# Kernel tuning notes

Hardware: AMD Instinct MI355X
Metric: run time of the kernel (lower is better)

Reference implementation:

```python
import jax, jax.numpy as jnp
import numpy as np

DIM = 1024
N_HEADS = 16
WINDOW = 256
B, N = 16, 4096
ACC = 512
EPS = 1e-5


def setup_inputs() -> dict:
    key = jax.random.key(0)
    ks = jax.random.split(key, 16)
    D = DIM
    sc = 1.0 / np.sqrt(D)
    inp = {
        "x": jax.random.normal(ks[0], (B, N, D), dtype=jnp.float32),
        "state": jax.random.normal(ks[1], (B, D), dtype=jnp.float32),
        "acc_ctx": jax.random.normal(ks[2], (B, ACC, D), dtype=jnp.float32),
        "fix_pt": jax.random.randint(ks[3], (B,), 0, N, dtype=jnp.int32),
        # MultiheadAttention params (torch layout: in_proj_weight [3D, D])
        "in_proj_w": jax.random.normal(ks[4], (3 * D, D), dtype=jnp.float32) * sc,
        "in_proj_b": jnp.zeros((3 * D,), dtype=jnp.float32),
        "out_w": jax.random.normal(ks[5], (D, D), dtype=jnp.float32) * sc,
        "out_b": jnp.zeros((D,), dtype=jnp.float32),
        # LayerNorms
        "ln1_g": jnp.ones((D,), dtype=jnp.float32),
        "ln1_b": jnp.zeros((D,), dtype=jnp.float32),
        "ln2_g": jnp.ones((D,), dtype=jnp.float32),
        "ln2_b": jnp.zeros((D,), dtype=jnp.float32),
        # FFN: dim -> 4*dim -> dim (stored so that y = x @ w + b)
        "w1": jax.random.normal(ks[6], (D, 4 * D), dtype=jnp.float32) * sc,
        "b1": jnp.zeros((4 * D,), dtype=jnp.float32),
        "w2": jax.random.normal(ks[7], (4 * D, D), dtype=jnp.float32) * (1.0 / np.sqrt(4 * D)),
        "b2": jnp.zeros((D,), dtype=jnp.float32),
    }
    return inp


def _layer_norm(x, g, b):
    m = jnp.mean(x, axis=-1, keepdims=True)
    v = jnp.mean(jnp.square(x - m), axis=-1, keepdims=True)
    return (x - m) * jax.lax.rsqrt(v + EPS) * g + b


def _extract_windows(x, fix_pt):
    # Vectorized equivalent of the per-sample python loop. For even window_size
    # and N >= window_size the original logic reduces to a clamped start index.
    half = WINDOW // 2
    n = x.shape[1]
    start = jnp.clip(fix_pt - half, 0, n - WINDOW)  # [B]
    idx = start[:, None] + jnp.arange(WINDOW)       # [B, W]
    return jnp.take_along_axis(x, idx[:, :, None], axis=1)  # [B, W, D]


def _mha(xq, in_proj_w, in_proj_b, out_w, out_b):
    # torch nn.MultiheadAttention self-attention, batch_first
    Bq, L, D = xq.shape
    hd = D // N_HEADS
    qkv = xq @ in_proj_w.T + in_proj_b                     # [B, L, 3D]
    q, k, v = jnp.split(qkv, 3, axis=-1)
    def heads(t):
        return t.reshape(Bq, L, N_HEADS, hd).transpose(0, 2, 1, 3)  # [B,H,L,hd]
    q, k, v = heads(q), heads(k), heads(v)
    scores = jnp.einsum('bhqd,bhkd->bhqk', q, k) / np.sqrt(hd)
    attn = jax.nn.softmax(scores, axis=-1)
    o = jnp.einsum('bhqk,bhkd->bhqd', attn, v)             # [B,H,L,hd]
    o = o.transpose(0, 2, 1, 3).reshape(Bq, L, D)
    return o @ out_w.T + out_b


def reference(x, state, acc_ctx, in_proj_w, in_proj_b, out_w, out_b,
              ln1_g, ln1_b, ln2_g, ln2_b, w1, b1, w2, b2, fix_pt):
    window = _extract_windows(x, fix_pt)                   # [B, W, D]
    cls = state[:, None, :]                                # [B, 1, D]
    ctx = jnp.concatenate([cls, acc_ctx, window], axis=1)  # [B, 1+A+W, D]
    normed = _layer_norm(ctx, ln1_g, ln1_b)
    out = _mha(normed, in_proj_w, in_proj_b, out_w, out_b)
    ctx = ctx + out
    cls_out = ctx[:, 0]
    h = jax.nn.gelu(_layer_norm(cls_out, ln2_g, ln2_b) @ w1 + b1, approximate=False)
    cls_out = cls_out + h @ w2 + b2
    new_acc = jnp.concatenate([acc_ctx, window], axis=1)
    return cls_out, new_acc
```

## Files before the change

kernel.cpp:

```cpp
#include <hip/hip_runtime.h>
#include <hip/hip_bf16.h>
#include <math.h>

#define DIM 1024
#define NHEADS 16
#define HD 64
#define WIN 256
#define NB 16
#define NSEQ 4096
#define NACC 512
#define LCTX 769
#define MROWS 12304
#define MPAD2 12544

typedef short bf16x8 __attribute__((ext_vector_type(8)));
typedef float f32x4 __attribute__((ext_vector_type(4)));

__device__ inline unsigned short f2b(float f) {
    union { float f; unsigned int u; } c; c.f = f;
    unsigned int u = c.u;
    u += 0x7FFFu + ((u >> 16) & 1u);
    return (unsigned short)(u >> 16);
}
__device__ inline float b2f(unsigned short h) {
    union { unsigned int u; float f; } c; c.u = ((unsigned int)h) << 16;
    return c.f;
}

__global__ __launch_bounds__(256) void build_ln_kernel(
    const float* __restrict__ x, const float* __restrict__ state,
    const float* __restrict__ acc_ctx, const int* __restrict__ fix_pt,
    const float* __restrict__ ln1_g, const float* __restrict__ ln1_b,
    const float* __restrict__ in_proj_w, unsigned short* __restrict__ Wb,
    unsigned short* __restrict__ normed, float* __restrict__ ctx0,
    float* __restrict__ newacc)
{
    int bid = blockIdx.x;
    int t = threadIdx.x;
    if (bid >= MPAD2) {
        int idx = (bid - MPAD2) * 256 + t;
        float4 v = ((const float4*)in_proj_w)[idx];
        ushort4 o;
        o.x = f2b(v.x); o.y = f2b(v.y); o.z = f2b(v.z); o.w = f2b(v.w);
        ((ushort4*)Wb)[idx] = o;
        return;
    }
    if (bid >= MROWS) {
        ushort4 z = make_ushort4(0, 0, 0, 0);
        ((ushort4*)(normed + (size_t)bid * DIM))[t] = z;
        return;
    }
    int b = bid / LCTX;
    int r = bid - b * LCTX;
    const float* src;
    if (r == 0) {
        src = state + (size_t)b * DIM;
    } else if (r <= NACC) {
        src = acc_ctx + ((size_t)b * NACC + (r - 1)) * DIM;
    } else {
        int fp = fix_pt[b];
        int start = fp - WIN / 2;
        if (start < 0) start = 0;
        if (start > NSEQ - WIN) start = NSEQ - WIN;
        src = x + ((size_t)b * NSEQ + start + (r - 1 - NACC)) * DIM;
    }
    float4 v = ((const float4*)src)[t];
    float s = v.x + v.y + v.z + v.w;
    float ss = v.x * v.x + v.y * v.y + v.z * v.z + v.w * v.w;
#pragma unroll
    for (int o = 32; o > 0; o >>= 1) { s += __shfl_down(s, o); ss += __shfl_down(ss, o); }
    __shared__ float rs[4], rss[4];
    int wid = t >> 6, lane = t & 63;
    if (lane == 0) { rs[wid] = s; rss[wid] = ss; }
    __syncthreads();
    float sum = rs[0] + rs[1] + rs[2] + rs[3];
    float sq  = rss[0] + rss[1] + rss[2] + rss[3];
    float mean = sum * (1.0f / DIM);
    float var = sq * (1.0f / DIM) - mean * mean;
    float rstd = rsqrtf(var + 1e-5f);
    float4 g  = ((const float4*)ln1_g)[t];
    float4 be = ((const float4*)ln1_b)[t];
    ushort4 nb;
    nb.x = f2b((v.x - mean) * rstd * g.x + be.x);
    nb.y = f2b((v.y - mean) * rstd * g.y + be.y);
    nb.z = f2b((v.z - mean) * rstd * g.z + be.z);
    nb.w = f2b((v.w - mean) * rstd * g.w + be.w);
    ((ushort4*)(normed + (size_t)bid * DIM))[t] = nb;
    if (r == 0) {
        ((float4*)(ctx0 + (size_t)b * DIM))[t] = v;
    } else {
        ((float4*)(newacc + ((size_t)b * (LCTX - 1) + (r - 1)) * DIM))[t] = v;
    }
}

__device__ inline void stage_half(const unsigned short* __restrict__ g,
                                  unsigned short* l, int t)
{
    {
        int r = t >> 3, c8 = (t & 7) ^ (r & 7);
        __builtin_amdgcn_global_load_lds(
            (const __attribute__((address_space(1))) void*)(g + (size_t)r * 1024 + c8 * 8),
            (__attribute__((address_space(3))) void*)(l + (size_t)t * 8), 16, 0, 0);
    }
    {
        int t2 = t + 512;
        int r = t2 >> 3, c8 = (t2 & 7) ^ (r & 7);
        __builtin_amdgcn_global_load_lds(
            (const __attribute__((address_space(1))) void*)(g + (size_t)r * 1024 + c8 * 8),
            (__attribute__((address_space(3))) void*)(l + (size_t)t2 * 8), 16, 0, 0);
    }
}

__device__ inline bf16x8 ldsw(const unsigned short* h, int r, int c8)
{
    int slot = r * 8 + (c8 ^ (r & 7));
    return *(const bf16x8*)(h + slot * 8);
}

__global__ __launch_bounds__(512, 2) void k_gemm8_kernel(
    const unsigned short* __restrict__ A,
    const unsigned short* __restrict__ Bw,
    const float* __restrict__ bias,
    unsigned short* __restrict__ C)
{
    __shared__ unsigned short sh[2][2][2][128 * 64];
    const int mt = blockIdx.x, nt = blockIdx.y;
    const int t = threadIdx.x;
    const int wid = t >> 6, lane = t & 63;
    const int wm = wid >> 2, wn = wid & 3;
    const int l15 = lane & 15, l16 = lane >> 4;
    const int rB = (wn & 1) * 64;
    const unsigned short* Abase = A + (size_t)mt * 256 * 1024;
    const unsigned short* Bbase = Bw + (size_t)nt * 256 * 1024;

    f32x4 acc[8][4] = {};
    bf16x8 a[4][2], b[4][2];

    stage_half(Abase,                   &sh[0][0][0][0], t);
    stage_half(Abase + 128 * 1024,      &sh[0][0][1][0], t);
    stage_half(Bbase,                   &sh[0][1][0][0], t);
    stage_half(Bbase + 128 * 1024,      &sh[0][1][1][0], t);
    stage_half(Bbase + 64,              &sh[1][1][0][0], t);
    stage_half(Bbase + 128 * 1024 + 64, &sh[1][1][1][0], t);
    asm volatile("s_waitcnt vmcnt(4)" ::: "memory");
    __builtin_amdgcn_s_barrier();

    auto ktile = [&](int T, bool stA, bool stB, bool steady) {
        const int d = T & 1;
        const unsigned short* AH = &sh[d][0][wm][0];
        const unsigned short* BH = &sh[d][1][wn >> 1][0];
        const int kA = (T + 1) * 64;
        const int kB = (T + 2) * 64;

#pragma unroll
        for (int i = 0; i < 4; ++i) {
            a[i][0] = ldsw(AH, i * 16 + l15, l16);
            a[i][1] = ldsw(AH, i * 16 + l15, 4 + l16);
        }
#pragma unroll
        for (int j = 0; j < 2; ++j) {
            b[j][0] = ldsw(BH, rB + j * 16 + l15, l16);
            b[j][1] = ldsw(BH, rB + j * 16 + l15, 4 + l16);
        }
        if (stA) stage_half(Abase + kA, &sh[d ^ 1][0][0][0], t);
        __builtin_amdgcn_sched_barrier(0);
        __builtin_amdgcn_s_barrier();
        asm volatile("s_waitcnt lgkmcnt(0)" ::: "memory");
        __builtin_amdgcn_sched_barrier(0);
        __builtin_amdgcn_s_setprio(1);
#pragma unroll
        for (int i = 0; i < 4; ++i)
#pragma unroll
            for (int j = 0; j < 2; ++j) {
                acc[i][j] = __builtin_amdgcn_mfma_f32_16x16x32_bf16(a[i][0], b[j][0], acc[i][j], 0, 0, 0);
                acc[i][j] = __builtin_amdgcn_mfma_f32_16x16x32_bf16(a[i][1], b[j][1], acc[i][j], 0, 0, 0);
            }
        __builtin_amdgcn_s_setprio(0);
        __builtin_amdgcn_sched_barrier(0);
        __builtin_amdgcn_s_barrier();

#pragma unroll
        for (int j = 2; j < 4; ++j) {
            b[j][0] = ldsw(BH, rB + j * 16 + l15, l16);
            b[j][1] = ldsw(BH, rB + j * 16 + l15, 4 + l16);
        }
        if (stA) stage_half(Abase + 128 * 1024 + kA, &sh[d ^ 1][0][1][0], t);
        __builtin_amdgcn_sched_barrier(0);
        __builtin_amdgcn_s_barrier();
        asm volatile("s_waitcnt lgkmcnt(0)" ::: "memory");
        __builtin_amdgcn_sched_barrier(0);
        __builtin_amdgcn_s_setprio(1);
#pragma unroll
        for (int i = 0; i < 4; ++i)
#pragma unroll
            for (int j = 2; j < 4; ++j) {
                acc[i][j] = __builtin_amdgcn_mfma_f32_16x16x32_bf16(a[i][0], b[j][0], acc[i][j], 0, 0, 0);
                acc[i][j] = __builtin_amdgcn_mfma_f32_16x16x32_bf16(a[i][1], b[j][1], acc[i][j], 0, 0, 0);
            }
        __builtin_amdgcn_s_setprio(0);
        __builtin_amdgcn_sched_barrier(0);
        __builtin_amdgcn_s_barrier();

#pragma unroll
        for (int i = 0; i < 4; ++i) {
            a[i][0] = ldsw(AH, 64 + i * 16 + l15, l16);
            a[i][1] = ldsw(AH, 64 + i * 16 + l15, 4 + l16);
        }
        if (stB) stage_half(Bbase + kB, &sh[d][1][0][0], t);
        __builtin_amdgcn_sched_barrier(0);
        __builtin_amdgcn_s_barrier();
        asm volatile("s_waitcnt lgkmcnt(0)" ::: "memory");
        __builtin_amdgcn_sched_barrier(0);
        __builtin_amdgcn_s_setprio(1);
#pragma unroll
        for (int i = 0; i < 4; ++i)
#pragma unroll
            for (int j = 0; j < 2; ++j) {
                acc[4 + i][j] = __builtin_amdgcn_mfma_f32_16x16x32_bf16(a[i][0], b[j][0], acc[4 + i][j], 0, 0, 0);
                acc[4 + i][j] = __builtin_amdgcn_mfma_f32_16x16x32_bf16(a[i][1], b[j][1], acc[4 + i][j], 0, 0, 0);
            }
        __builtin_amdgcn_s_setprio(0);
        __builtin_amdgcn_sched_barrier(0);
        __builtin_amdgcn_s_barrier();

        if (stB) stage_half(Bbase + 128 * 1024 + kB, &sh[d][1][1][0], t);
        __builtin_amdgcn_sched_barrier(0);
        __builtin_amdgcn_s_barrier();
        asm volatile("s_waitcnt lgkmcnt(0)" ::: "memory");
        __builtin_amdgcn_sched_barrier(0);
        __builtin_amdgcn_s_setprio(1);
#pragma unroll
        for (int i = 0; i < 4; ++i)
#pragma unroll
            for (int j = 2; j < 4; ++j) {
                acc[4 + i][j] = __builtin_amdgcn_mfma_f32_16x16x32_bf16(a[i][0], b[j][0], acc[4 + i][j], 0, 0, 0);
                acc[4 + i][j] = __builtin_amdgcn_mfma_f32_16x16x32_bf16(a[i][1], b[j][1], acc[4 + i][j], 0, 0, 0);
            }
        __builtin_amdgcn_s_setprio(0);
        if (steady) {
            asm volatile("s_waitcnt vmcnt(4)" ::: "memory");
        } else {
            asm volatile("s_waitcnt vmcnt(0)" ::: "memory");
        }
        __builtin_amdgcn_sched_barrier(0);
        __builtin_amdgcn_s_barrier();
    };

    for (int T = 0; T < 14; ++T) ktile(T, true, true, true);
    ktile(14, true, false, false);
    ktile(15, false, false, false);

#pragma unroll
    for (int i = 0; i < 8; ++i) {
        int gmb = mt * 256 + wm * 128 + i * 16 + l16 * 4;
#pragma unroll
        for (int j = 0; j < 4; ++j) {
            int gn = nt * 256 + wn * 64 + j * 16 + l15;
            float bs = bias[gn];
#pragma unroll
            for (int r = 0; r < 4; ++r) {
                int gm = gmb + r;
                if (gm < MROWS) C[(size_t)gm * 1024 + gn] = f2b(acc[i][j][r] + bs);
            }
        }
    }
}

__global__ __launch_bounds__(512) void attn3_kernel(
    const unsigned short* __restrict__ normed,
    const unsigned short* __restrict__ Wqb, const float* __restrict__ in_proj_w,
    const float* __restrict__ in_proj_b,
    const unsigned short* __restrict__ kb, float* __restrict__ o_all)
{
    int b = blockIdx.x & 15, h = blockIdx.x >> 4;
    int t = threadIdx.x;
    int wave = t >> 6, lane = t & 63;
    __shared__ float qs[64];
    __shared__ float sc[LCTX];
    __shared__ float red1[8], red2[8];
    __shared__ float c4[4][1024];
    __shared__ float cfin[1024];

    {
        const unsigned short* nr = normed + (size_t)(b * LCTX) * DIM;
        bf16x8 n0 = *(const bf16x8*)(nr + lane * 16);
        bf16x8 n1 = *(const bf16x8*)(nr + lane * 16 + 8);
#pragma unroll
        for (int jj = 0; jj < 8; ++jj) {
            int d = wave * 8 + jj;
            const unsigned short* wr = Wqb + (size_t)(h * 64 + d) * DIM;
            bf16x8 w0 = *(const bf16x8*)(wr + lane * 16);
            bf16x8 w1 = *(const bf16x8*)(wr + lane * 16 + 8);
            float s = 0.f;
#pragma unroll
            for (int u = 0; u < 8; ++u)
                s += b2f((unsigned short)n0[u]) * b2f((unsigned short)w0[u]);
#pragma unroll
            for (int u = 0; u < 8; ++u)
                s += b2f((unsigned short)n1[u]) * b2f((unsigned short)w1[u]);
#pragma unroll
            for (int o = 32; o > 0; o >>= 1) s += __shfl_down(s, o);
            if (lane == 0) qs[d] = s + in_proj_b[h * 64 + d];
        }
    }
    __syncthreads();

    float lmax = -1e30f;
    for (int l = t; l < LCTX; l += 512) {
        const unsigned short* kr = kb + ((size_t)(b * LCTX + l)) * 1024 + h * 64;
        const uint4* k4 = (const uint4*)kr;
        float s = 0.f;
#pragma unroll
        for (int c = 0; c < 8; ++c) {
            uint4 u = k4[c];
            s += qs[c * 8 + 0] * b2f((unsigned short)(u.x & 0xffffu));
            s += qs[c * 8 + 1] * b2f((unsigned short)(u.x >> 16));
            s += qs[c * 8 + 2] * b2f((unsigned short)(u.y & 0xffffu));
            s += qs[c * 8 + 3] * b2f((unsigned short)(u.y >> 16));
            s += qs[c * 8 + 4] * b2f((unsigned short)(u.z & 0xffffu));
            s += qs[c * 8 + 5] * b2f((unsigned short)(u.z >> 16));
            s += qs[c * 8 + 6] * b2f((unsigned short)(u.w & 0xffffu));
            s += qs[c * 8 + 7] * b2f((unsigned short)(u.w >> 16));
        }
        s *= 0.125f;
        sc[l] = s;
        lmax = fmaxf(lmax, s);
    }
#pragma unroll
    for (int o = 32; o > 0; o >>= 1) lmax = fmaxf(lmax, __shfl_down(lmax, o));
    if (lane == 0) red1[wave] = lmax;
    __syncthreads();
    float m = red1[0];
#pragma unroll
    for (int w8 = 1; w8 < 8; ++w8) m = fmaxf(m, red1[w8]);

    float lsum = 0.f;
    for (int l = t; l < LCTX; l += 512) {
        float p = __expf(sc[l] - m);
        sc[l] = p;
        lsum += p;
    }
#pragma unroll
    for (int o = 32; o > 0; o >>= 1) lsum += __shfl_down(lsum, o);
    if (lane == 0) red2[wave] = lsum;
    __syncthreads();
    float S = 0.f;
#pragma unroll
    for (int w8 = 0; w8 < 8; ++w8) S += red2[w8];

    const unsigned short* nb_ = normed + (size_t)(b * LCTX) * DIM;
    int oc = t & 127;
    int rg = t >> 7;
    float ca[8] = {};
    for (int l = rg; l < LCTX; l += 4) {
        bf16x8 v = *(const bf16x8*)(nb_ + (size_t)l * DIM + oc * 8);
        float p = sc[l];
#pragma unroll
        for (int u = 0; u < 8; ++u) ca[u] += p * b2f((unsigned short)v[u]);
    }
#pragma unroll
    for (int u = 0; u < 8; ++u) c4[rg][oc * 8 + u] = ca[u];
    __syncthreads();
    for (int k = t; k < 1024; k += 512)
        cfin[k] = c4[0][k] + c4[1][k] + c4[2][k] + c4[3][k];
    __syncthreads();

    float rS = 1.0f / S;
#pragma unroll
    for (int dd = 0; dd < 8; ++dd) {
        int d = wave * 8 + dd;
        const float* wr = in_proj_w + (size_t)(2048 + h * 64 + d) * DIM;
        float s = 0.f;
#pragma unroll
        for (int kk = 0; kk < 16; ++kk) {
            int k = kk * 64 + lane;
            s += wr[k] * cfin[k];
        }
#pragma unroll
        for (int o = 32; o > 0; o >>= 1) s += __shfl_down(s, o);
        if (lane == 0)
            o_all[b * 1024 + h * 64 + d] = s * rS + in_proj_b[2048 + h * 64 + d];
    }
}

__global__ __launch_bounds__(256) void out_proj_kernel(
    const float* __restrict__ o_all, const float* __restrict__ out_w,
    const float* __restrict__ out_b, const float* __restrict__ ctx0,
    float* __restrict__ cls_pre)
{
    int gw = blockIdx.x * 4 + (threadIdx.x >> 6);
    int lane = threadIdx.x & 63;
    int b = gw >> 10, i = gw & 1023;
    const float* orow = o_all + (size_t)b * 1024;
    const float* wrow = out_w + (size_t)i * 1024;
    float s = 0.f;
#pragma unroll
    for (int kk = 0; kk < 16; ++kk) {
        int k = kk * 64 + lane;
        s += orow[k] * wrow[k];
    }
#pragma unroll
    for (int o = 32; o > 0; o >>= 1) s += __shfl_down(s, o);
    if (lane == 0) cls_pre[gw] = ctx0[gw] + s + out_b[i];
}

__global__ __launch_bounds__(256) void ln2_kernel(
    const float* __restrict__ cls_pre, const float* __restrict__ g,
    const float* __restrict__ be, const float* __restrict__ b2,
    float* __restrict__ ln2o, float* __restrict__ outp)
{
    int b = blockIdx.x, t = threadIdx.x;
    float4 v = ((const float4*)(cls_pre + (size_t)b * DIM))[t];
    float s = v.x + v.y + v.z + v.w;
    float ss = v.x * v.x + v.y * v.y + v.z * v.z + v.w * v.w;
#pragma unroll
    for (int o = 32; o > 0; o >>= 1) { s += __shfl_down(s, o); ss += __shfl_down(ss, o); }
    __shared__ float rs[4], rss[4];
    int wid = t >> 6, lane = t & 63;
    if (lane == 0) { rs[wid] = s; rss[wid] = ss; }
    __syncthreads();
    float sum = rs[0] + rs[1] + rs[2] + rs[3];
    float sq  = rss[0] + rss[1] + rss[2] + rss[3];
    float mean = sum * (1.0f / DIM);
    float var = sq * (1.0f / DIM) - mean * mean;
    float rstd = rsqrtf(var + 1e-5f);
    float4 gv = ((const float4*)g)[t];
    float4 bv = ((const float4*)be)[t];
    float4 o;
    o.x = (v.x - mean) * rstd * gv.x + bv.x;
    o.y = (v.y - mean) * rstd * gv.y + bv.y;
    o.z = (v.z - mean) * rstd * gv.z + bv.z;
    o.w = (v.w - mean) * rstd * gv.w + bv.w;
    ((float4*)(ln2o + (size_t)b * DIM))[t] = o;
    float4 b2v = ((const float4*)b2)[t];
    float4 oi;
    oi.x = v.x + b2v.x; oi.y = v.y + b2v.y; oi.z = v.z + b2v.z; oi.w = v.w + b2v.w;
    ((float4*)(outp + (size_t)b * DIM))[t] = oi;
}

__global__ __launch_bounds__(256) void mlp1p_kernel(
    const float* __restrict__ ln2v, const float* __restrict__ w1,
    float* __restrict__ part)
{
    __shared__ float l2s[16][256];
    __shared__ float red[4][64][16];
    int jc = blockIdx.x, kq = blockIdx.y;
    int t = threadIdx.x;
#pragma unroll
    for (int b = 0; b < 16; ++b)
        l2s[b][t] = ln2v[(size_t)b * 1024 + kq * 256 + t];
    __syncthreads();
    int jl = t & 63, ks = t >> 6;
    int j = jc * 64 + jl;
    float acc[16] = {};
    for (int kk = 0; kk < 64; ++kk) {
        int kl = ks * 64 + kk;
        float wv = w1[(size_t)(kq * 256 + kl) * 4096 + j];
#pragma unroll
        for (int b = 0; b < 16; ++b) acc[b] += l2s[b][kl] * wv;
    }
#pragma unroll
    for (int b = 0; b < 16; ++b) red[ks][jl][b] = acc[b];
    __syncthreads();
    int jl2 = t & 63, bq = t >> 6;
#pragma unroll
    for (int bb = 0; bb < 4; ++bb) {
        int b = bq * 4 + bb;
        float s = red[0][jl2][b] + red[1][jl2][b] + red[2][jl2][b] + red[3][jl2][b];
        part[((size_t)kq * 16 + b) * 4096 + jc * 64 + jl2] = s;
    }
}

__global__ __launch_bounds__(256) void mlp2a_kernel(
    const float* __restrict__ part, const float* __restrict__ b1,
    const float* __restrict__ w2, float* __restrict__ outp)
{
    __shared__ float hseg[16][256];
    __shared__ float red[4][64][16];
    int ic = blockIdx.x, kq = blockIdx.y;
    int t = threadIdx.x;
    {
        int j = kq * 256 + t;
        float bb1 = b1[j];
#pragma unroll
        for (int b = 0; b < 16; ++b) {
            float s = part[((size_t)0 * 16 + b) * 4096 + j]
                    + part[((size_t)1 * 16 + b) * 4096 + j]
                    + part[((size_t)2 * 16 + b) * 4096 + j]
                    + part[((size_t)3 * 16 + b) * 4096 + j];
            s += bb1;
            hseg[b][t] = 0.5f * s * (1.0f + erff(s * 0.70710678118f));
        }
    }
    __syncthreads();
    int il = t & 63, ks = t >> 6;
    int i = ic * 64 + il;
    float acc[16] = {};
    for (int kk = 0; kk < 64; ++kk) {
        int kl = ks * 64 + kk;
        float wv = w2[(size_t)(kq * 256 + kl) * 1024 + i];
#pragma unroll
        for (int b = 0; b < 16; ++b) acc[b] += hseg[b][kl] * wv;
    }
#pragma unroll
    for (int b = 0; b < 16; ++b) red[ks][il][b] = acc[b];
    __syncthreads();
    int il2 = t & 63, bq = t >> 6;
#pragma unroll
    for (int bb = 0; bb < 4; ++bb) {
        int b = bq * 4 + bb;
        float s = red[0][il2][b] + red[1][il2][b] + red[2][il2][b] + red[3][il2][b];
        atomicAdd(&outp[(size_t)b * 1024 + ic * 64 + il2], s);
    }
}

extern "C" void kernel_launch(void* const* d_in, const int* in_sizes, int n_in,
                              void* d_out, int out_size, void* d_ws, size_t ws_size,
                              hipStream_t stream)
{
    const float* x        = (const float*)d_in[0];
    const float* state    = (const float*)d_in[1];
    const float* acc_ctx  = (const float*)d_in[2];
    const int*   fix_pt   = (const int*)d_in[3];
    const float* in_proj_w = (const float*)d_in[4];
    const float* in_proj_b = (const float*)d_in[5];
    const float* out_w    = (const float*)d_in[6];
    const float* out_b    = (const float*)d_in[7];
    const float* ln1_g    = (const float*)d_in[8];
    const float* ln1_b    = (const float*)d_in[9];
    const float* ln2_g    = (const float*)d_in[10];
    const float* ln2_b    = (const float*)d_in[11];
    const float* w1       = (const float*)d_in[12];
    const float* b1       = (const float*)d_in[13];
    const float* w2       = (const float*)d_in[14];
    const float* b2       = (const float*)d_in[15];
    float* outp = (float*)d_out;

    char* ws = (char*)d_ws;
    unsigned short* normed = (unsigned short*)ws; ws += (size_t)MPAD2 * DIM * 2;
    unsigned short* Wb     = (unsigned short*)ws; ws += (size_t)2048 * DIM * 2;
    unsigned short* kb     = (unsigned short*)ws; ws += (size_t)MROWS * 1024 * 2;
    float* ctx0    = (float*)ws; ws += (size_t)NB * DIM * 4;
    float* o_all   = (float*)ws; ws += (size_t)NB * DIM * 4;
    float* cls_pre = (float*)ws; ws += (size_t)NB * DIM * 4;
    float* ln2v    = (float*)ws; ws += (size_t)NB * DIM * 4;
    float* part    = (float*)ws; ws += (size_t)4 * 16 * 4096 * 4;

    float* newacc = outp + (size_t)NB * DIM;

    hipLaunchKernelGGL(build_ln_kernel, dim3(MPAD2 + 2048), dim3(256), 0, stream,
                       x, state, acc_ctx, fix_pt, ln1_g, ln1_b,
                       in_proj_w, Wb, normed, ctx0, newacc);
    hipLaunchKernelGGL(k_gemm8_kernel, dim3(49, 4), dim3(512), 0, stream,
                       normed, Wb + (size_t)1024 * DIM, in_proj_b + 1024, kb);
    hipLaunchKernelGGL(attn3_kernel, dim3(256), dim3(512), 0, stream,
                       normed, Wb, in_proj_w, in_proj_b, kb, o_all);
    hipLaunchKernelGGL(out_proj_kernel, dim3(4096), dim3(256), 0, stream,
                       o_all, out_w, out_b, ctx0, cls_pre);
    hipLaunchKernelGGL(ln2_kernel, dim3(16), dim3(256), 0, stream,
                       cls_pre, ln2_g, ln2_b, b2, ln2v, outp);
    hipLaunchKernelGGL(mlp1p_kernel, dim3(64, 4), dim3(256), 0, stream,
                       ln2v, w1, part);
    hipLaunchKernelGGL(mlp2a_kernel, dim3(16, 16), dim3(256), 0, stream,
                       part, b1, w2, outp);
}
```

Before: 174.1 us.

## Split attention into score, context and V-projection kernels sharing normed reads across heads

```diff
diff --git a/kernel.cpp b/kernel.cpp
--- a/kernel.cpp
+++ b/kernel.cpp
@@ -12,6 +12,7 @@
 #define LCTX 769
 #define MROWS 12304
 #define MPAD2 12544
+#define PSTR 772
 
 typedef short bf16x8 __attribute__((ext_vector_type(8)));
 typedef float f32x4 __attribute__((ext_vector_type(4)));
@@ -266,11 +267,10 @@
     }
 }
 
-__global__ __launch_bounds__(512) void attn3_kernel(
+__global__ __launch_bounds__(512) void score_kernel(
     const unsigned short* __restrict__ normed,
-    const unsigned short* __restrict__ Wqb, const float* __restrict__ in_proj_w,
-    const float* __restrict__ in_proj_b,
-    const unsigned short* __restrict__ kb, float* __restrict__ o_all)
+    const unsigned short* __restrict__ Wqb, const float* __restrict__ in_proj_b,
+    const unsigned short* __restrict__ kb, float* __restrict__ ps)
 {
     int b = blockIdx.x & 15, h = blockIdx.x >> 4;
     int t = threadIdx.x;
@@ -278,8 +278,6 @@
     __shared__ float qs[64];
     __shared__ float sc[LCTX];
     __shared__ float red1[8], red2[8];
-    __shared__ float c4[4][1024];
-    __shared__ float cfin[1024];
 
     {
         const unsigned short* nr = normed + (size_t)(b * LCTX) * DIM;
@@ -347,40 +345,59 @@
     float S = 0.f;
 #pragma unroll
     for (int w8 = 0; w8 < 8; ++w8) S += red2[w8];
-
-    const unsigned short* nb_ = normed + (size_t)(b * LCTX) * DIM;
-    int oc = t & 127;
-    int rg = t >> 7;
-    float ca[8] = {};
-    for (int l = rg; l < LCTX; l += 4) {
-        bf16x8 v = *(const bf16x8*)(nb_ + (size_t)l * DIM + oc * 8);
-        float p = sc[l];
-#pragma unroll
-        for (int u = 0; u < 8; ++u) ca[u] += p * b2f((unsigned short)v[u]);
-    }
-#pragma unroll
-    for (int u = 0; u < 8; ++u) c4[rg][oc * 8 + u] = ca[u];
-    __syncthreads();
-    for (int k = t; k < 1024; k += 512)
-        cfin[k] = c4[0][k] + c4[1][k] + c4[2][k] + c4[3][k];
-    __syncthreads();
-
     float rS = 1.0f / S;
-#pragma unroll
-    for (int dd = 0; dd < 8; ++dd) {
-        int d = wave * 8 + dd;
-        const float* wr = in_proj_w + (size_t)(2048 + h * 64 + d) * DIM;
-        float s = 0.f;
-#pragma unroll
-        for (int kk = 0; kk < 16; ++kk) {
-            int k = kk * 64 + lane;
-            s += wr[k] * cfin[k];
-        }
-#pragma unroll
-        for (int o = 32; o > 0; o >>= 1) s += __shfl_down(s, o);
-        if (lane == 0)
-            o_all[b * 1024 + h * 64 + d] = s * rS + in_proj_b[2048 + h * 64 + d];
-    }
+
+    float* po = ps + (size_t)(b * 16 + h) * PSTR;
+    for (int l = t; l < LCTX; l += 512) po[l] = sc[l] * rS;
+}
+
+__global__ __launch_bounds__(256) void ctx_kernel(
+    const unsigned short* __restrict__ normed, const float* __restrict__ ps,
+    float* __restrict__ c_all)
+{
+    int cc = blockIdx.x, b = blockIdx.y;
+    int t = threadIdx.x;
+    __shared__ float pl[16][PSTR];
+
+    for (int h = 0; h < 16; ++h)
+        for (int l = t; l < LCTX; l += 256)
+            pl[h][l] = ps[(size_t)(b * 16 + h) * PSTR + l];
+    __syncthreads();
+
+    int oct = t & 15;
+    int h = t >> 4;
+    const unsigned short* nb_ = normed + (size_t)(b * LCTX) * DIM + cc * 128 + oct * 8;
+    float acc[8] = {};
+    for (int l = 0; l < LCTX; ++l) {
+        bf16x8 v = *(const bf16x8*)(nb_ + (size_t)l * DIM);
+        float p = pl[h][l];
+#pragma unroll
+        for (int u = 0; u < 8; ++u) acc[u] += p * b2f((unsigned short)v[u]);
+    }
+    float* co = c_all + (size_t)(b * 16 + h) * 1024 + cc * 128 + oct * 8;
+#pragma unroll
+    for (int u = 0; u < 8; ++u) co[u] = acc[u];
+}
+
+__global__ __launch_bounds__(256) void vproj_kernel(
+    const float* __restrict__ c_all, const float* __restrict__ in_proj_w,
+    const float* __restrict__ in_proj_b, float* __restrict__ o_all)
+{
+    int gw = blockIdx.x * 4 + (threadIdx.x >> 6);
+    int lane = threadIdx.x & 63;
+    int b = gw >> 10, j = gw & 1023;
+    int h = j >> 6;
+    const float* crow = c_all + (size_t)(b * 16 + h) * 1024;
+    const float* wrow = in_proj_w + (size_t)(2048 + j) * DIM;
+    float s = 0.f;
+#pragma unroll
+    for (int kk = 0; kk < 16; ++kk) {
+        int k = kk * 64 + lane;
+        s += crow[k] * wrow[k];
+    }
+#pragma unroll
+    for (int o = 32; o > 0; o >>= 1) s += __shfl_down(s, o);
+    if (lane == 0) o_all[gw] = s + in_proj_b[2048 + j];
 }
 
 __global__ __launch_bounds__(256) void out_proj_kernel(
@@ -540,6 +557,8 @@
     unsigned short* normed = (unsigned short*)ws; ws += (size_t)MPAD2 * DIM * 2;
     unsigned short* Wb     = (unsigned short*)ws; ws += (size_t)2048 * DIM * 2;
     unsigned short* kb     = (unsigned short*)ws; ws += (size_t)MROWS * 1024 * 2;
+    float* ps      = (float*)ws; ws += (size_t)NB * NHEADS * PSTR * 4;
+    float* c_all   = (float*)ws; ws += (size_t)NB * NHEADS * 1024 * 4;
     float* ctx0    = (float*)ws; ws += (size_t)NB * DIM * 4;
     float* o_all   = (float*)ws; ws += (size_t)NB * DIM * 4;
     float* cls_pre = (float*)ws; ws += (size_t)NB * DIM * 4;
@@ -553,8 +572,12 @@
                        in_proj_w, Wb, normed, ctx0, newacc);
     hipLaunchKernelGGL(k_gemm8_kernel, dim3(49, 4), dim3(512), 0, stream,
                        normed, Wb + (size_t)1024 * DIM, in_proj_b + 1024, kb);
-    hipLaunchKernelGGL(attn3_kernel, dim3(256), dim3(512), 0, stream,
-                       normed, Wb, in_proj_w, in_proj_b, kb, o_all);
+    hipLaunchKernelGGL(score_kernel, dim3(256), dim3(512), 0, stream,
+                       normed, Wb, in_proj_b, kb, ps);
+    hipLaunchKernelGGL(ctx_kernel, dim3(8, 16), dim3(256), 0, stream,
+                       normed, ps, c_all);
+    hipLaunchKernelGGL(vproj_kernel, dim3(4096), dim3(256), 0, stream,
+                       c_all, in_proj_w, in_proj_b, o_all);
     hipLaunchKernelGGL(out_proj_kernel, dim3(4096), dim3(256), 0, stream,
                        o_all, out_w, out_b, ctx0, cls_pre);
     hipLaunchKernelGGL(ln2_kernel, dim3(16), dim3(256), 0, stream,
```

Result: slower. 270.5 us (+55.4%).
